# Kernel tuning notes

Measured on AMD Instinct MI355X. Metric: run time of the kernel, lower is better.

## Reference

```python
import jax, jax.numpy as jnp
import numpy as np

DIM = 192
HEADS = 8
EPS = 1e-12  # torch F.normalize eps


def setup_inputs() -> dict:
    key = jax.random.key(0)
    ks = jax.random.split(key, 6)
    b, c, h, w = 8, DIM, 128, 128
    x = jax.random.normal(ks[0], (b, c, h, w), dtype=jnp.float32)
    feature = jax.random.normal(ks[1], (b, c, h, w), dtype=jnp.float32)
    # Conv2d(dim, 3*dim, 1, bias=False) -> weight (3*dim, dim, 1, 1); store squeezed (3*dim, dim)
    W_qkv = jax.random.normal(ks[2], (3 * c, c), dtype=jnp.float32) * (1.0 / np.sqrt(c))
    # Depthwise Conv2d(3*dim, 3*dim, 3, padding=1, groups=3*dim) -> weight (3*dim, 1, 3, 3)
    W_dw = jax.random.normal(ks[3], (3 * c, 1, 3, 3), dtype=jnp.float32) * (1.0 / 3.0)
    # Conv2d(dim, dim, 1, bias=False) -> (dim, dim)
    W_proj = jax.random.normal(ks[4], (c, c), dtype=jnp.float32) * (1.0 / np.sqrt(c))
    temperature = jnp.ones((HEADS, 1, 1), dtype=jnp.float32)
    return {"x": x, "feature": feature, "W_qkv": W_qkv, "W_dw": W_dw,
            "W_proj": W_proj, "temperature": temperature}


def _l2_normalize(t):
    # torch F.normalize(dim=-1): t / max(||t||_2, eps)
    n = jnp.sqrt(jnp.sum(t * t, axis=-1, keepdims=True))
    return t / jnp.maximum(n, EPS)


def reference(x, feature, W_qkv, W_dw, W_proj, temperature):
    b, c, h, w = x.shape
    head = HEADS
    ch = c // head  # channels per head
    # 1x1 conv (pointwise): bchw,oc -> bohw
    qkv = jnp.einsum('bchw,oc->bohw', x, W_qkv)
    # 3x3 depthwise conv, padding=1
    qkv = jax.lax.conv_general_dilated(
        qkv, W_dw, window_strides=(1, 1), padding=((1, 1), (1, 1)),
        dimension_numbers=('NCHW', 'OIHW', 'NCHW'), feature_group_count=3 * c)
    q, k, v = jnp.split(qkv, 3, axis=1)
    # b (head ch) h w -> b head ch (h w)
    q = q.reshape(b, head, ch, h * w)
    k = k.reshape(b, head, ch, h * w)
    v = v.reshape(b, head, ch, h * w)
    f = feature.reshape(b, head, ch, h * w)
    q = _l2_normalize(q * f)
    k = _l2_normalize(k * f)
    # small c x c attention per (batch, head)
    attn = jnp.einsum('bhcn,bhdn->bhcd', q, k) * temperature
    attn = jax.nn.softmax(attn, axis=-1)
    out = jnp.einsum('bhcd,bhdn->bhcn', attn, v)
    out = out.reshape(b, c, h, w)
    out = jnp.einsum('bchw,oc->bohw', out, W_proj)
    return out
```

## Files before the change

### kernel.cpp

```cpp
#include <hip/hip_runtime.h>

typedef unsigned short u16;
typedef short s16x8 __attribute__((ext_vector_type(8)));
typedef float f32x4 __attribute__((ext_vector_type(4)));

__device__ __forceinline__ float bf2f(u16 u) {
  return __uint_as_float(((unsigned)u) << 16);
}
__device__ __forceinline__ u16 f2bf(float f) {
  unsigned x = __float_as_uint(f);
  return (u16)((x + 0x7fffu + ((x >> 16) & 1u)) >> 16);
}

__global__ __launch_bounds__(256) void wcvt_k(
    const float* __restrict__ W, u16* __restrict__ Wb)
{
  const int i = (blockIdx.x * 256 + threadIdx.x) * 8;
  const float4 f0 = *(const float4*)(W + i);
  const float4 f1 = *(const float4*)(W + i + 4);
  union { s16x8 v; u16 u[8]; } pk;
  pk.u[0]=f2bf(f0.x); pk.u[1]=f2bf(f0.y); pk.u[2]=f2bf(f0.z); pk.u[3]=f2bf(f0.w);
  pk.u[4]=f2bf(f1.x); pk.u[5]=f2bf(f1.y); pk.u[6]=f2bf(f1.z); pk.u[7]=f2bf(f1.w);
  *(s16x8*)(Wb + i) = pk.v;
}

__global__ __launch_bounds__(256, 3) void qkv_fused(
    const float* __restrict__ x, const u16* __restrict__ Wb,
    u16* __restrict__ qkv)
{
  __shared__ u16 xs[128*200];
  const int t = threadIdx.x, wave = t >> 6, lane = t & 63;
  const int l15 = lane & 15, l4 = lane >> 4;
  const int p0 = blockIdx.x * 128, b = blockIdx.y;

  const float* const xb = x + (long)b*192*16384 + p0;
  #pragma unroll
  for (int i = 0; i < 24; i++) {
    const int idx = t + i*256;
    const int c = idx >> 5, p4 = (idx & 31) * 4;
    const float4 v = *(const float4*)(xb + (long)c*16384 + p4);
    xs[(p4+0)*200 + c] = f2bf(v.x);
    xs[(p4+1)*200 + c] = f2bf(v.y);
    xs[(p4+2)*200 + c] = f2bf(v.z);
    xs[(p4+3)*200 + c] = f2bf(v.w);
  }
  __syncthreads();

  const int ocH = (wave >> 1) * 288, pH = (wave & 1) * 64;
  u16* const qb = qkv + (long)b*576*16384 + p0 + pH;

  auto loadW = [&](s16x8 (&af)[2][6], int oc0) {
    #pragma unroll
    for (int ni = 0; ni < 2; ni++)
      #pragma unroll
      for (int kq = 0; kq < 6; kq++)
        af[ni][kq] = *(const s16x8*)(Wb + (long)(oc0 + ni*16 + l15)*192 + kq*32 + l4*8);
  };

  s16x8 afA[2][6], afB[2][6];
  loadW(afA, ocH);

  #pragma unroll
  for (int ot = 0; ot < 9; ot++) {
    s16x8 (&afc)[2][6] = (ot & 1) ? afB : afA;
    s16x8 (&afn)[2][6] = (ot & 1) ? afA : afB;
    if (ot < 8) loadW(afn, ocH + (ot+1)*32);

    f32x4 acc[2][4];
    #pragma unroll
    for (int ni = 0; ni < 2; ni++)
      #pragma unroll
      for (int mi = 0; mi < 4; mi++) acc[ni][mi] = (f32x4){0.f,0.f,0.f,0.f};

    #pragma unroll
    for (int kq = 0; kq < 6; kq++) {
      s16x8 bx[4];
      #pragma unroll
      for (int mi = 0; mi < 4; mi++)
        bx[mi] = *(const s16x8*)(xs + (pH + mi*16 + l15)*200 + kq*32 + l4*8);
      #pragma unroll
      for (int ni = 0; ni < 2; ni++)
        #pragma unroll
        for (int mi = 0; mi < 4; mi++)
          acc[ni][mi] = __builtin_amdgcn_mfma_f32_16x16x32_bf16(
              afc[ni][kq], bx[mi], acc[ni][mi], 0, 0, 0);
    }

    #pragma unroll
    for (int ni = 0; ni < 2; ni++)
      #pragma unroll
      for (int mi = 0; mi < 4; mi++) {
        const int p = mi*16 + l15;
        #pragma unroll
        for (int j = 0; j < 4; j++) {
          const int row = ocH + ot*32 + ni*16 + l4*4 + j;
          qb[(long)row*16384 + p] = f2bf(acc[ni][mi][j]);
        }
      }
  }
}

__global__ __launch_bounds__(256, 3) void proj_fused(
    const u16* __restrict__ qkv, const u16* __restrict__ M2,
    float* __restrict__ outp)
{
  __shared__ u16 vs[128*200];
  const int t = threadIdx.x, wave = t >> 6, lane = t & 63;
  const int l15 = lane & 15, l4 = lane >> 4;
  const int p0 = blockIdx.x * 128, b = blockIdx.y;

  const u16* const vb = qkv + ((long)b*576 + 384)*16384 + p0;
  #pragma unroll
  for (int i = 0; i < 12; i++) {
    const int idx = t + i*256;
    const int g = idx >> 4, p8 = (idx & 15) * 8;
    union { s16x8 v; u16 u[8]; } ld;
    ld.v = *(const s16x8*)(vb + (long)g*16384 + p8);
    #pragma unroll
    for (int j = 0; j < 8; j++) vs[(p8+j)*200 + g] = ld.u[j];
  }
  __syncthreads();

  const int ocH = (wave >> 1) * 96, pH = (wave & 1) * 64;
  const u16* const Mb = M2 + (long)b * 36864;
  float* const ob = outp + (long)b*192*16384 + p0 + pH;

  auto loadA = [&](s16x8 (&af)[2][6], int oc0) {
    #pragma unroll
    for (int ni = 0; ni < 2; ni++)
      #pragma unroll
      for (int kq = 0; kq < 6; kq++)
        af[ni][kq] = *(const s16x8*)(Mb + (long)(oc0 + ni*16 + l15)*192 + kq*32 + l4*8);
  };

  s16x8 afA[2][6], afB[2][6];
  loadA(afA, ocH);

  #pragma unroll
  for (int ot = 0; ot < 3; ot++) {
    s16x8 (&afc)[2][6] = (ot & 1) ? afB : afA;
    s16x8 (&afn)[2][6] = (ot & 1) ? afA : afB;
    if (ot < 2) loadA(afn, ocH + (ot+1)*32);

    f32x4 acc[2][4];
    #pragma unroll
    for (int ni = 0; ni < 2; ni++)
      #pragma unroll
      for (int mi = 0; mi < 4; mi++) acc[ni][mi] = (f32x4){0.f,0.f,0.f,0.f};

    #pragma unroll
    for (int kq = 0; kq < 6; kq++) {
      s16x8 bx[4];
      #pragma unroll
      for (int mi = 0; mi < 4; mi++)
        bx[mi] = *(const s16x8*)(vs + (pH + mi*16 + l15)*200 + kq*32 + l4*8);
      #pragma unroll
      for (int ni = 0; ni < 2; ni++)
        #pragma unroll
        for (int mi = 0; mi < 4; mi++)
          acc[ni][mi] = __builtin_amdgcn_mfma_f32_16x16x32_bf16(
              afc[ni][kq], bx[mi], acc[ni][mi], 0, 0, 0);
    }

    #pragma unroll
    for (int ni = 0; ni < 2; ni++)
      #pragma unroll
      for (int mi = 0; mi < 4; mi++) {
        const int p = mi*16 + l15;
        #pragma unroll
        for (int j = 0; j < 4; j++) {
          const int row = ocH + ot*32 + ni*16 + l4*4 + j;
          ob[(long)row*16384 + p] = acc[ni][mi][j];
        }
      }
  }
}

__global__ __launch_bounds__(256) void dwconv_k(
    u16* __restrict__ qkv, const float* __restrict__ Wdw)
{
  __shared__ u16 lds[130*132];
  const int ch = blockIdx.x, b = blockIdx.y;
  u16* const base = qkv + ((long)b * 576 + ch) * 16384;
  const int t = threadIdx.x;

  {
    uint4* z = (uint4*)lds;
    #pragma unroll
    for (int i = 0; i < 9; i++) {
      const int idx = t + i*256;
      if (idx < 2145) z[idx] = (uint4){0,0,0,0};
    }
  }
  float w[9];
  #pragma unroll
  for (int i = 0; i < 9; i++) w[i] = Wdw[ch*9 + i];
  __syncthreads();

  #pragma unroll
  for (int i = 0; i < 8; i++) {
    const int p = t + i*256;
    const int y = p >> 4, x = (p & 15) * 8;
    union { uint4 v; u16 u[8]; } ld;
    ld.v = *(const uint4*)(base + y*128 + x);
    u16* d = &lds[(y+1)*132 + x + 1];
    #pragma unroll
    for (int kk = 0; kk < 8; kk++) d[kk] = ld.u[kk];
  }
  __syncthreads();

  #pragma unroll
  for (int i = 0; i < 8; i++) {
    const int p = t + i*256;
    const int y = p >> 4, x = (p & 15) * 8;
    float r[3][10];
    #pragma unroll
    for (int dy = 0; dy < 3; dy++)
      #pragma unroll
      for (int j = 0; j < 10; j++)
        r[dy][j] = bf2f(lds[(y+dy)*132 + x + j]);
    float acc[8];
    #pragma unroll
    for (int xx = 0; xx < 8; xx++)
      acc[xx] = w[0]*r[0][xx] + w[1]*r[0][xx+1] + w[2]*r[0][xx+2]
              + w[3]*r[1][xx] + w[4]*r[1][xx+1] + w[5]*r[1][xx+2]
              + w[6]*r[2][xx] + w[7]*r[2][xx+1] + w[8]*r[2][xx+2];
    union { uint4 v; u16 u[8]; } st;
    #pragma unroll
    for (int xx = 0; xx < 8; xx++) st.u[xx] = f2bf(acc[xx]);
    *(uint4*)(base + y*128 + x) = st.v;
  }
}

__global__ __launch_bounds__(256) void gram_k(
    const u16* __restrict__ qkv, const float* __restrict__ feature,
    float* __restrict__ Gp)
{
  __shared__ u16 us[48*128];
  __shared__ float red[4*2304];
  const int kc = blockIdx.x, bh = blockIdx.y;
  const int b = bh >> 3, h = bh & 7;
  const int t = threadIdx.x, wave = t >> 6, lane = t & 63;
  const int l15 = lane & 15, l4 = lane >> 4;
  const u16* const qbase = qkv + ((long)b*576 + h*24) * 16384;
  const u16* const kbase = qkv + ((long)b*576 + 192 + h*24) * 16384;
  const float* const fbase = feature + ((long)b*192 + h*24) * 16384;
  char* const usb = (char*)us;

  f32x4 acc[3][3];
  #pragma unroll
  for (int i = 0; i < 3; i++)
    #pragma unroll
    for (int j = 0; j < 3; j++) acc[i][j] = (f32x4){0.f, 0.f, 0.f, 0.f};

  for (int step = 0; step < 16; step++) {
    const int k0 = kc*2048 + step*128;
    #pragma unroll
    for (int i = 0; i < 3; i++) {
      const int idx = t + i*256;
      const int r = idx >> 5, d4 = idx & 31;
      const long po = (long)r*16384 + k0 + d4*4;
      const float4 f4 = *(const float4*)(fbase + po);
      union { uint2 v; u16 u[4]; } uq, uk, oq, ok;
      uq.v = *(const uint2*)(qbase + po);
      uk.v = *(const uint2*)(kbase + po);
      const float fv[4] = {f4.x, f4.y, f4.z, f4.w};
      #pragma unroll
      for (int j = 0; j < 4; j++) {
        oq.u[j] = f2bf(bf2f(uq.u[j]) * fv[j]);
        ok.u[j] = f2bf(bf2f(uk.u[j]) * fv[j]);
      }
      const int col = d4*4;
      const int sub = ((col&7)<<1);
      const int r2 = r + 24;
      *(uint2*)(usb + r *256 + (((col>>3) ^ (r &7)) << 4) + sub) = oq.v;
      *(uint2*)(usb + r2*256 + (((col>>3) ^ (r2&7)) << 4) + sub) = ok.v;
    }
    __syncthreads();
    {
      const int kb = wave*4 + l4;
      s16x8 fr[3];
      #pragma unroll
      for (int g = 0; g < 3; g++) {
        const int row = g*16 + l15;
        fr[g] = *(const s16x8*)(usb + row*256 + ((kb ^ (row&7)) << 4));
      }
      #pragma unroll
      for (int gm = 0; gm < 3; gm++)
        #pragma unroll
        for (int gn = 0; gn < 3; gn++)
          acc[gm][gn] = __builtin_amdgcn_mfma_f32_16x16x32_bf16(fr[gm], fr[gn], acc[gm][gn], 0, 0, 0);
    }
    __syncthreads();
  }
  #pragma unroll
  for (int gm = 0; gm < 3; gm++)
    #pragma unroll
    for (int gn = 0; gn < 3; gn++)
      #pragma unroll
      for (int j = 0; j < 4; j++) {
        const int r = gm*16 + l4*4 + j, s = gn*16 + l15;
        red[wave*2304 + r*48 + s] = acc[gm][gn][j];
      }
  __syncthreads();
  for (int idx = t; idx < 2304; idx += 256) {
    const float sum = red[idx] + red[2304+idx] + red[4608+idx] + red[6912+idx];
    Gp[((long)bh*8 + kc)*2304 + idx] = sum;
  }
}

__global__ __launch_bounds__(256) void attnfin_k(
    const float* __restrict__ Gp, const float* __restrict__ temperature,
    float* __restrict__ attn)
{
  __shared__ float cross[576];
  __shared__ float qn[24], kn[24];
  const int bh = blockIdx.x, h = bh & 7;
  const int t = threadIdx.x;
  const float* const g = Gp + (long)bh * 8 * 2304;
  for (int idx = t; idx < 624; idx += 256) {
    float s = 0.f;
    if (idx < 576) {
      const int c = idx / 24, d = idx - c * 24;
      #pragma unroll
      for (int kc = 0; kc < 8; kc++) s += g[kc*2304 + c*48 + 24 + d];
      cross[idx] = s;
    } else {
      const int r = idx - 576;
      #pragma unroll
      for (int kc = 0; kc < 8; kc++) s += g[kc*2304 + r*48 + r];
      const float nv = fmaxf(sqrtf(s), 1e-12f);
      if (r < 24) qn[r] = nv; else kn[r-24] = nv;
    }
  }
  __syncthreads();
  if (t < 24) {
    const float tmp = temperature[h];
    const float qi = 1.f / qn[t];
    float vals[24];
    float m = -1e30f;
    #pragma unroll
    for (int d = 0; d < 24; d++) {
      const float v = cross[t*24 + d] * qi / kn[d] * tmp;
      vals[d] = v; m = fmaxf(m, v);
    }
    float s = 0.f;
    #pragma unroll
    for (int d = 0; d < 24; d++) { vals[d] = __expf(vals[d] - m); s += vals[d]; }
    const float inv = 1.f / s;
    #pragma unroll
    for (int d = 0; d < 24; d++) attn[(long)bh*576 + t*24 + d] = vals[d] * inv;
  }
}

__global__ __launch_bounds__(256) void m2_k(
    const float* __restrict__ attn, const float* __restrict__ Wp,
    u16* __restrict__ M2)
{
  const int gid = blockIdx.x * 256 + threadIdx.x;
  const int g = gid % 192;
  const int rem = gid / 192;
  const int o = rem % 192;
  const int b = rem / 192;
  const int h = g / 24, d = g - h*24;
  const float* a = attn + ((long)(b*8 + h) * 24) * 24 + d;
  const float* w = Wp + (long)o * 192 + h * 24;
  float s = 0.f;
  #pragma unroll
  for (int c = 0; c < 24; c++) s += w[c] * a[c*24];
  M2[gid] = f2bf(s);
}

extern "C" void kernel_launch(void* const* d_in, const int* in_sizes, int n_in,
                              void* d_out, int out_size, void* d_ws, size_t ws_size,
                              hipStream_t stream) {
  const float* x    = (const float*)d_in[0];
  const float* fe   = (const float*)d_in[1];
  const float* Wqkv = (const float*)d_in[2];
  const float* Wdw  = (const float*)d_in[3];
  const float* Wpr  = (const float*)d_in[4];
  const float* temp = (const float*)d_in[5];

  char* ws = (char*)d_ws;
  u16*   qkv = (u16*)ws;
  float* Gp  = (float*)(ws + 150994944L);
  float* attn= (float*)(ws + 155713536L);
  u16*   M2  = (u16*)(ws + 155860992L);
  u16*   Wb  = (u16*)(ws + 156450816L);

  wcvt_k<<<54, 256, 0, stream>>>(Wqkv, Wb);
  qkv_fused<<<dim3(128,8), 256, 0, stream>>>(x, Wb, qkv);
  dwconv_k<<<dim3(576,8), 256, 0, stream>>>(qkv, Wdw);
  gram_k<<<dim3(8,64), 256, 0, stream>>>(qkv, fe, Gp);
  attnfin_k<<<64, 256, 0, stream>>>(Gp, temp, attn);
  m2_k<<<1152, 256, 0, stream>>>(attn, Wpr, M2);
  proj_fused<<<dim3(128,8), 256, 0, stream>>>(qkv, M2, (float*)d_out);
}
```

Measured before the change: 251.5 us.

## Halve pixel tile in qkv/proj GEMMs, drop weight double-buffering, swizzle LDS transpose stores

The pointwise-conv GEMM kernels (qkv_fused and proj_fused) now process 64 pixels per block instead of 128, which doubles the grid and halves LDS use. The register double-buffered weight fragments are replaced with per-k-step loads, which lowers register pressure and raises occupancy. The LDS transpose stores are rotated by lane (and packed as two channels per 32-bit word in qkv) to reduce bank conflicts. In exchange, each block reuses every weight fragment across fewer pixels, so weight global/L2 traffic per output rises, and the weight-load latency is no longer prefetched.

```diff
diff --git a/kernel.cpp b/kernel.cpp
--- a/kernel.cpp
+++ b/kernel.cpp
@@ -24,155 +24,142 @@
   *(s16x8*)(Wb + i) = pk.v;
 }
 
-__global__ __launch_bounds__(256, 3) void qkv_fused(
+__global__ __launch_bounds__(256) void qkv_fused(
     const float* __restrict__ x, const u16* __restrict__ Wb,
     u16* __restrict__ qkv)
 {
-  __shared__ u16 xs[128*200];
+  __shared__ u16 xs[64*200];
   const int t = threadIdx.x, wave = t >> 6, lane = t & 63;
   const int l15 = lane & 15, l4 = lane >> 4;
-  const int p0 = blockIdx.x * 128, b = blockIdx.y;
+  const int p0 = blockIdx.x * 64, b = blockIdx.y;
 
   const float* const xb = x + (long)b*192*16384 + p0;
   #pragma unroll
-  for (int i = 0; i < 24; i++) {
+  for (int i = 0; i < 6; i++) {
     const int idx = t + i*256;
-    const int c = idx >> 5, p4 = (idx & 31) * 4;
-    const float4 v = *(const float4*)(xb + (long)c*16384 + p4);
-    xs[(p4+0)*200 + c] = f2bf(v.x);
-    xs[(p4+1)*200 + c] = f2bf(v.y);
-    xs[(p4+2)*200 + c] = f2bf(v.z);
-    xs[(p4+3)*200 + c] = f2bf(v.w);
-  }
-  __syncthreads();
-
-  const int ocH = (wave >> 1) * 288, pH = (wave & 1) * 64;
+    const int cp = idx >> 4, quad = idx & 15;
+    const int c = cp*2, p4 = quad*4;
+    const float4 f0 = *(const float4*)(xb + (long)c*16384 + p4);
+    const float4 f1 = *(const float4*)(xb + (long)(c+1)*16384 + p4);
+    const float a0[4] = {f0.x, f0.y, f0.z, f0.w};
+    const float a1[4] = {f1.x, f1.y, f1.z, f1.w};
+    #pragma unroll
+    for (int j = 0; j < 4; j++) {
+      const int jj = (j + quad) & 3;
+      const unsigned v = (unsigned)f2bf(a0[jj]) | ((unsigned)f2bf(a1[jj]) << 16);
+      *(unsigned*)(&xs[(p4 + jj)*200 + c]) = v;
+    }
+  }
+  __syncthreads();
+
+  const int ocH = (wave >> 1) * 288, pH = (wave & 1) * 32;
   u16* const qb = qkv + (long)b*576*16384 + p0 + pH;
 
-  auto loadW = [&](s16x8 (&af)[2][6], int oc0) {
-    #pragma unroll
-    for (int ni = 0; ni < 2; ni++)
-      #pragma unroll
-      for (int kq = 0; kq < 6; kq++)
-        af[ni][kq] = *(const s16x8*)(Wb + (long)(oc0 + ni*16 + l15)*192 + kq*32 + l4*8);
-  };
-
-  s16x8 afA[2][6], afB[2][6];
-  loadW(afA, ocH);
-
-  #pragma unroll
   for (int ot = 0; ot < 9; ot++) {
-    s16x8 (&afc)[2][6] = (ot & 1) ? afB : afA;
-    s16x8 (&afn)[2][6] = (ot & 1) ? afA : afB;
-    if (ot < 8) loadW(afn, ocH + (ot+1)*32);
-
-    f32x4 acc[2][4];
-    #pragma unroll
-    for (int ni = 0; ni < 2; ni++)
-      #pragma unroll
-      for (int mi = 0; mi < 4; mi++) acc[ni][mi] = (f32x4){0.f,0.f,0.f,0.f};
+    const int oc0 = ocH + ot*32;
+    f32x4 acc[2][2];
+    #pragma unroll
+    for (int mi = 0; mi < 2; mi++)
+      #pragma unroll
+      for (int ni = 0; ni < 2; ni++) acc[mi][ni] = (f32x4){0.f,0.f,0.f,0.f};
 
     #pragma unroll
     for (int kq = 0; kq < 6; kq++) {
-      s16x8 bx[4];
-      #pragma unroll
-      for (int mi = 0; mi < 4; mi++)
+      s16x8 wf[2], bx[2];
+      #pragma unroll
+      for (int ni = 0; ni < 2; ni++)
+        wf[ni] = *(const s16x8*)(Wb + (long)(oc0 + ni*16 + l15)*192 + kq*32 + l4*8);
+      #pragma unroll
+      for (int mi = 0; mi < 2; mi++)
         bx[mi] = *(const s16x8*)(xs + (pH + mi*16 + l15)*200 + kq*32 + l4*8);
       #pragma unroll
-      for (int ni = 0; ni < 2; ni++)
-        #pragma unroll
-        for (int mi = 0; mi < 4; mi++)
-          acc[ni][mi] = __builtin_amdgcn_mfma_f32_16x16x32_bf16(
-              afc[ni][kq], bx[mi], acc[ni][mi], 0, 0, 0);
-    }
-
-    #pragma unroll
-    for (int ni = 0; ni < 2; ni++)
-      #pragma unroll
-      for (int mi = 0; mi < 4; mi++) {
-        const int p = mi*16 + l15;
+      for (int mi = 0; mi < 2; mi++)
+        #pragma unroll
+        for (int ni = 0; ni < 2; ni++)
+          acc[mi][ni] = __builtin_amdgcn_mfma_f32_16x16x32_bf16(
+              wf[ni], bx[mi], acc[mi][ni], 0, 0, 0);
+    }
+
+    #pragma unroll
+    for (int mi = 0; mi < 2; mi++) {
+      const int p = mi*16 + l15;
+      #pragma unroll
+      for (int ni = 0; ni < 2; ni++) {
         #pragma unroll
         for (int j = 0; j < 4; j++) {
-          const int row = ocH + ot*32 + ni*16 + l4*4 + j;
-          qb[(long)row*16384 + p] = f2bf(acc[ni][mi][j]);
+          const int row = oc0 + ni*16 + l4*4 + j;
+          qb[(long)row*16384 + p] = f2bf(acc[mi][ni][j]);
         }
       }
-  }
-}
-
-__global__ __launch_bounds__(256, 3) void proj_fused(
+    }
+  }
+}
+
+__global__ __launch_bounds__(256) void proj_fused(
     const u16* __restrict__ qkv, const u16* __restrict__ M2,
     float* __restrict__ outp)
 {
-  __shared__ u16 vs[128*200];
+  __shared__ u16 vs[64*200];
   const int t = threadIdx.x, wave = t >> 6, lane = t & 63;
   const int l15 = lane & 15, l4 = lane >> 4;
-  const int p0 = blockIdx.x * 128, b = blockIdx.y;
+  const int p0 = blockIdx.x * 64, b = blockIdx.y;
 
   const u16* const vb = qkv + ((long)b*576 + 384)*16384 + p0;
   #pragma unroll
-  for (int i = 0; i < 12; i++) {
+  for (int i = 0; i < 6; i++) {
     const int idx = t + i*256;
-    const int g = idx >> 4, p8 = (idx & 15) * 8;
+    const int g = idx >> 3, oct = idx & 7;
     union { s16x8 v; u16 u[8]; } ld;
-    ld.v = *(const s16x8*)(vb + (long)g*16384 + p8);
-    #pragma unroll
-    for (int j = 0; j < 8; j++) vs[(p8+j)*200 + g] = ld.u[j];
-  }
-  __syncthreads();
-
-  const int ocH = (wave >> 1) * 96, pH = (wave & 1) * 64;
+    ld.v = *(const s16x8*)(vb + (long)g*16384 + oct*8);
+    #pragma unroll
+    for (int j = 0; j < 8; j++) {
+      const int jj = (j + oct) & 7;
+      vs[(oct*8 + jj)*200 + g] = ld.u[jj];
+    }
+  }
+  __syncthreads();
+
+  const int ocH = (wave >> 1) * 96, pH = (wave & 1) * 32;
   const u16* const Mb = M2 + (long)b * 36864;
   float* const ob = outp + (long)b*192*16384 + p0 + pH;
 
-  auto loadA = [&](s16x8 (&af)[2][6], int oc0) {
-    #pragma unroll
-    for (int ni = 0; ni < 2; ni++)
-      #pragma unroll
-      for (int kq = 0; kq < 6; kq++)
-        af[ni][kq] = *(const s16x8*)(Mb + (long)(oc0 + ni*16 + l15)*192 + kq*32 + l4*8);
-  };
-
-  s16x8 afA[2][6], afB[2][6];
-  loadA(afA, ocH);
-
-  #pragma unroll
   for (int ot = 0; ot < 3; ot++) {
-    s16x8 (&afc)[2][6] = (ot & 1) ? afB : afA;
-    s16x8 (&afn)[2][6] = (ot & 1) ? afA : afB;
-    if (ot < 2) loadA(afn, ocH + (ot+1)*32);
-
-    f32x4 acc[2][4];
-    #pragma unroll
-    for (int ni = 0; ni < 2; ni++)
-      #pragma unroll
-      for (int mi = 0; mi < 4; mi++) acc[ni][mi] = (f32x4){0.f,0.f,0.f,0.f};
+    const int oc0 = ocH + ot*32;
+    f32x4 acc[2][2];
+    #pragma unroll
+    for (int mi = 0; mi < 2; mi++)
+      #pragma unroll
+      for (int ni = 0; ni < 2; ni++) acc[mi][ni] = (f32x4){0.f,0.f,0.f,0.f};
 
     #pragma unroll
     for (int kq = 0; kq < 6; kq++) {
-      s16x8 bx[4];
-      #pragma unroll
-      for (int mi = 0; mi < 4; mi++)
+      s16x8 wf[2], bx[2];
+      #pragma unroll
+      for (int ni = 0; ni < 2; ni++)
+        wf[ni] = *(const s16x8*)(Mb + (long)(oc0 + ni*16 + l15)*192 + kq*32 + l4*8);
+      #pragma unroll
+      for (int mi = 0; mi < 2; mi++)
         bx[mi] = *(const s16x8*)(vs + (pH + mi*16 + l15)*200 + kq*32 + l4*8);
       #pragma unroll
-      for (int ni = 0; ni < 2; ni++)
-        #pragma unroll
-        for (int mi = 0; mi < 4; mi++)
-          acc[ni][mi] = __builtin_amdgcn_mfma_f32_16x16x32_bf16(
-              afc[ni][kq], bx[mi], acc[ni][mi], 0, 0, 0);
-    }
-
-    #pragma unroll
-    for (int ni = 0; ni < 2; ni++)
-      #pragma unroll
-      for (int mi = 0; mi < 4; mi++) {
-        const int p = mi*16 + l15;
+      for (int mi = 0; mi < 2; mi++)
+        #pragma unroll
+        for (int ni = 0; ni < 2; ni++)
+          acc[mi][ni] = __builtin_amdgcn_mfma_f32_16x16x32_bf16(
+              wf[ni], bx[mi], acc[mi][ni], 0, 0, 0);
+    }
+
+    #pragma unroll
+    for (int mi = 0; mi < 2; mi++) {
+      const int p = mi*16 + l15;
+      #pragma unroll
+      for (int ni = 0; ni < 2; ni++) {
         #pragma unroll
         for (int j = 0; j < 4; j++) {
-          const int row = ocH + ot*32 + ni*16 + l4*4 + j;
-          ob[(long)row*16384 + p] = acc[ni][mi][j];
+          const int row = oc0 + ni*16 + l4*4 + j;
+          ob[(long)row*16384 + p] = acc[mi][ni][j];
         }
       }
+    }
   }
 }
 
@@ -389,10 +376,10 @@
   u16*   Wb  = (u16*)(ws + 156450816L);
 
   wcvt_k<<<54, 256, 0, stream>>>(Wqkv, Wb);
-  qkv_fused<<<dim3(128,8), 256, 0, stream>>>(x, Wb, qkv);
+  qkv_fused<<<dim3(256,8), 256, 0, stream>>>(x, Wb, qkv);
   dwconv_k<<<dim3(576,8), 256, 0, stream>>>(qkv, Wdw);
   gram_k<<<dim3(8,64), 256, 0, stream>>>(qkv, fe, Gp);
   attnfin_k<<<64, 256, 0, stream>>>(Gp, temp, attn);
   m2_k<<<1152, 256, 0, stream>>>(attn, Wpr, M2);
-  proj_fused<<<dim3(128,8), 256, 0, stream>>>(qkv, M2, (float*)d_out);
-}
+  proj_fused<<<dim3(256,8), 256, 0, stream>>>(qkv, M2, (float*)d_out);
+}
```

After: 311.5 us. +23.8%, slower.
